# Performance work log

Hardware: AMD Instinct MI355X
Metric: run time of the kernel (lower is better)

Reference implementation:

```python
import jax, jax.numpy as jnp
import numpy as np

M, C, D_EMB, K, LBP_LOOPS, DAMP = 100, 30, 300, 3, 10, 0.5


def setup_inputs() -> dict:
    key = jax.random.key(0)
    k0, k1, k2, k3, k4, k5 = jax.random.split(key, 6)
    ent = jax.random.normal(k0, (M, C, D_EMB), jnp.float32)
    fmc_in = jax.random.normal(k1, (M, 3 * D_EMB), jnp.float32)
    W_fmc = jax.random.normal(k2, (3 * D_EMB, D_EMB), jnp.float32) / np.float32(np.sqrt(3 * D_EMB))
    b_fmc = jnp.zeros((D_EMB,), jnp.float32)
    eye = jnp.eye(D_EMB, dtype=jnp.float32)
    # original init: B, R_k, D_k are identity (diag of ones); add tiny noise so grads are generic
    B = eye + 0.01 * jax.random.normal(k3, (D_EMB, D_EMB), jnp.float32)
    R = eye[None] + 0.01 * jax.random.normal(k4, (K, D_EMB, D_EMB), jnp.float32)
    D = eye[None] + 0.01 * jax.random.normal(k5, (K, D_EMB, D_EMB), jnp.float32)
    return {"ent": ent, "fmc_in": fmc_in, "W_fmc": W_fmc, "b_fmc": b_fmc, "B": B, "R": R, "D": D}


def _lbp(ent, fmc_in, W_fmc, b_fmc, B, R, D):
    # f_m_c: Linear(900,300) + Tanh (dropout off in eval)
    f = jnp.tanh(fmc_in @ W_fmc + b_fmc)                              # [M, d]
    # psi(e, m) = e^T B f_c(m)
    psi = jnp.einsum('mcd,de,me->mc', ent, B, f)                      # [M, C]
    # a_k(m_i, m_j) = softmax_k( f_i^T D_k f_j / sqrt(d) )  (RelNorm)
    s = jnp.einsum('id,kde,je->ijk', f, D, f) / np.float32(np.sqrt(D_EMB))
    a = jax.nn.softmax(s, axis=-1)                                    # [M, M, K]
    # phi_ks(arg, e')_k = arg^T R_k e'  ; arg = candidate q of mention j, e' = candidate p of mention i
    pk = jnp.einsum('jqd,kde,ipe->ijpqk', ent, R, ent)                # [M, M, C, C, K]
    phi = jnp.einsum('ijpqk,ijk->ijpq', pk, a)                        # [M, M, C(e'), C(arg)]

    mbar0 = jnp.zeros((M, M, C), jnp.float32)                         # mbar[i, j, arg-of-j]

    def step(mbar, _):
        stot = mbar.sum(axis=0)                                       # sum_k mbar[k, i, e']  -> [M, C]
        # value(i, j, e'=p, arg=q) = psi(e', i) + phi(arg, e', i, j) + sum_{k != j} mbar[k, i, e']
        vals = (psi[:, None, :, None] + phi
                + stot[:, None, :, None]
                - jnp.transpose(mbar, (1, 0, 2))[:, :, :, None])      # subtract k == j term
        mval = jnp.maximum(0.0, vals.max(axis=2))                     # max over e', maxValue init 0
        # damped update in prob space: log((1-g)*exp(mbar) + g*softmax_arg(mval))
        new = jnp.log((1.0 - DAMP) * jnp.exp(mbar)
                      + DAMP * jax.nn.softmax(mval, axis=-1))
        return new, None

    mbar, _ = jax.lax.scan(step, mbar0, None, length=LBP_LOOPS)

    # ubar[i, arg] = softmax_arg( psi(arg, i) + sum_{k != i} mbar[k, i, arg] )
    u = psi + mbar.sum(axis=0) - jnp.einsum('iic->ic', mbar)
    return jax.nn.softmax(u, axis=-1)                                 # [M, C]


def reference(ent, fmc_in, W_fmc, b_fmc, B, R, D):
    return _lbp(ent, fmc_in, W_fmc, b_fmc, B, R, D)
```

## Files before the change

### kernel.cpp

```cpp
#include <hip/hip_runtime.h>
#include <math.h>

#define MM 100
#define CC 30
#define DE 300
#define NK 3
#define NLOOP 10
#define INV_SQRT_D 0.05773502691896258f

typedef __attribute__((ext_vector_type(8))) short bf16x8;
typedef __attribute__((ext_vector_type(4))) float f32x4;


__device__ inline void bf16split(float x, short* hi, short* lo) {
  unsigned u  = __float_as_uint(x);
  unsigned hu = u & 0xFFFF0000u;
  float xh = __uint_as_float(hu);
  float rl = x - xh;
  unsigned lu = __float_as_uint(rl);
  lu += 0x7FFFu + ((lu >> 16) & 1u);
  *hi = (short)(hu >> 16);
  *lo = (short)(lu >> 16);
}

__global__ __launch_bounds__(256) void k_f1(const float* __restrict__ fmc,
                                            const float* __restrict__ W,
                                            const float* __restrict__ b,
                                            float* __restrict__ f) {
  __shared__ float xs[75];
  const int m  = blockIdx.x / 12;
  const int eq = blockIdx.x % 12;
  const int e0 = eq * 75;
  const int tid = threadIdx.x;
  for (int e = tid; e < 75; e += 256) xs[e] = fmc[m*3*DE + e0 + e];
  __syncthreads();

  const int d0 = tid;
  const int d1 = tid + 256;
  float acc0 = 0.f, acc1 = 0.f;
  for (int e = 0; e < 75; ++e) {
    const float xv = xs[e];
    const float* Wr = W + (e0 + e)*DE;
    acc0 = fmaf(xv, Wr[d0], acc0);
    if (d1 < DE) acc1 = fmaf(xv, Wr[d1], acc1);
  }
  if (eq == 0) {
    acc0 += b[d0];
    if (d1 < DE) acc1 += b[d1];
  }
  atomicAdd(f + m*DE + d0, acc0);
  if (d1 < DE) atomicAdd(f + m*DE + d1, acc1);
}

__global__ void k_tanh(float* __restrict__ f, int n) {
  int idx = blockIdx.x*256 + threadIdx.x;
  if (idx < n) f[idx] = tanhf(f[idx]);
}

__global__ __launch_bounds__(256) void k_gt(const float* __restrict__ Bm,
                                            const float* __restrict__ Dm,
                                            const float* __restrict__ f,
                                            float* __restrict__ gst,
                                            float* __restrict__ t) {
  __shared__ float fs[DE];
  const int m  = blockIdx.x / 19;
  const int cg = blockIdx.x % 19;
  const int wave = threadIdx.x >> 6, lane = threadIdx.x & 63;
  for (int e = threadIdx.x; e < DE; e += 256) fs[e] = f[m*DE + e];
  __syncthreads();

  #pragma unroll
  for (int u = 0; u < 16; ++u) {
    const int col = cg*64 + wave*16 + u;
    const bool ok = (col < 1200);
    const int ccl = ok ? col : 0;
    const float* row = (ccl < DE) ? (Bm + ccl*DE) : (Dm + (ccl - DE)*DE);
    float acc = 0.f;
    for (int e = lane; e < DE; e += 64) acc = fmaf(row[e], fs[e], acc);
    #pragma unroll
    for (int off = 32; off; off >>= 1) acc += __shfl_down(acc, off, 64);
    if (ok && lane == 0) {
      if (col < DE) {
        gst[m*DE + col] = acc;
      } else {
        const int k = (col - DE) / DE, d = (col - DE) % DE;
        t[(k*MM + m)*DE + d] = acc;
      }
    }
  }
}

__global__ __launch_bounds__(256) void k_psi2(const float* __restrict__ ent,
                                              const float* __restrict__ gst,
                                              float* __restrict__ psi) {
  __shared__ float gs[DE];
  const int m  = blockIdx.x >> 3;
  const int cg = blockIdx.x & 7;
  const int wave = threadIdx.x >> 6, lane = threadIdx.x & 63;
  for (int e = threadIdx.x; e < DE; e += 256) gs[e] = gst[m*DE + e];
  __syncthreads();
  const int c = cg*4 + wave;
  if (c < CC) {
    float acc = 0.f;
    const float* er = ent + (m*CC + c)*DE;
    for (int d = lane; d < DE; d += 64) acc = fmaf(er[d], gs[d], acc);
    #pragma unroll
    for (int off = 32; off; off >>= 1) acc += __shfl_down(acc, off, 64);
    if (lane == 0) psi[m*CC + c] = acc;
  }
}

__global__ __launch_bounds__(256) void k_a2(const float* __restrict__ f,
                                            const float* __restrict__ t,
                                            float* __restrict__ a) {
  __shared__ float fs[DE];
  const int i  = blockIdx.x / 25;
  const int jg = blockIdx.x % 25;
  const int wave = threadIdx.x >> 6, lane = threadIdx.x & 63;
  for (int e = threadIdx.x; e < DE; e += 256) fs[e] = f[i*DE + e];
  __syncthreads();
  const int j = jg*4 + wave;
  float sk[NK];
  #pragma unroll
  for (int k = 0; k < NK; ++k) {
    float acc = 0.f;
    const float* tr = t + (k*MM + j)*DE;
    for (int d = lane; d < DE; d += 64) acc = fmaf(fs[d], tr[d], acc);
    #pragma unroll
    for (int off = 32; off; off >>= 1) acc += __shfl_down(acc, off, 64);
    sk[k] = acc;
  }
  if (lane == 0) {
    float s0 = sk[0]*INV_SQRT_D, s1 = sk[1]*INV_SQRT_D, s2 = sk[2]*INV_SQRT_D;
    float mx = fmaxf(s0, fmaxf(s1, s2));
    float e0 = expf(s0 - mx), e1 = expf(s1 - mx), e2 = expf(s2 - mx);
    float inv = 1.f / (e0 + e1 + e2);
    float* ar = a + (i*MM + j)*NK;
    ar[0] = e0*inv; ar[1] = e1*inv; ar[2] = e2*inv;
  }
}

__global__ __launch_bounds__(256) void k_esplit(const float* __restrict__ ent,
                                                short* __restrict__ entH,
                                                short* __restrict__ entL) {
  int j = blockIdx.x;
  for (int idx = threadIdx.x; idx < 32*320; idx += 256) {
    int q = idx / 320, kk = idx % 320;
    float x = (q < CC && kk < DE) ? ent[(j*CC + q)*DE + kk] : 0.f;
    short h, l;
    bf16split(x, &h, &l);
    entH[(j*32 + q)*320 + kk] = h;
    entL[(j*32 + q)*320 + kk] = l;
  }
}

__global__ __launch_bounds__(256) void k_re(const float* __restrict__ R,
                                            const float* __restrict__ ent,
                                            short* __restrict__ REH,
                                            short* __restrict__ REL) {
  __shared__ float4 As4[128*5];
  __shared__ float4 Bs4[64*5];
  float* As = (float*)As4;
  float* Bs = (float*)Bs4;

  const int k  = blockIdx.z;
  const int r0 = blockIdx.y * 128;
  const int d0 = blockIdx.x * 64;
  const int tx = threadIdx.x & 15;
  const int ty = threadIdx.x >> 4;
  const float* A  = ent;
  const float* Bk = R + k*DE*DE;

  float acc[8][4];
  #pragma unroll
  for (int r = 0; r < 8; ++r)
    #pragma unroll
    for (int s = 0; s < 4; ++s) acc[r][s] = 0.f;

  for (int e0 = 0; e0 < DE; e0 += 20) {
    #pragma unroll
    for (int it = 0; it < 10; ++it) {
      int idx = threadIdx.x + it*256;
      int row = idx / 20, e = idx % 20;
      int gr = r0 + row;
      As[idx] = (gr < MM*CC) ? A[gr*DE + e0 + e] : 0.f;
    }
    #pragma unroll
    for (int it = 0; it < 5; ++it) {
      int idx = threadIdx.x + it*256;
      int row = idx / 20, e = idx % 20;
      int gd = d0 + row;
      Bs[idx] = (gd < DE) ? Bk[gd*DE + e0 + e] : 0.f;
    }
    __syncthreads();

    #pragma unroll
    for (int v = 0; v < 5; ++v) {
      float4 av[8], bv[4];
      #pragma unroll
      for (int r = 0; r < 8; ++r) av[r] = As4[(ty + 16*r)*5 + v];
      #pragma unroll
      for (int s = 0; s < 4; ++s) bv[s] = Bs4[(tx + 16*s)*5 + v];
      #pragma unroll
      for (int r = 0; r < 8; ++r)
        #pragma unroll
        for (int s = 0; s < 4; ++s) {
          acc[r][s] = fmaf(av[r].x, bv[s].x, acc[r][s]);
          acc[r][s] = fmaf(av[r].y, bv[s].y, acc[r][s]);
          acc[r][s] = fmaf(av[r].z, bv[s].z, acc[r][s]);
          acc[r][s] = fmaf(av[r].w, bv[s].w, acc[r][s]);
        }
    }
    __syncthreads();
  }

  #pragma unroll
  for (int r = 0; r < 8; ++r) {
    int gr = r0 + ty + 16*r;
    if (gr < MM*CC) {
      int i = gr / CC, p = gr % CC;
      #pragma unroll
      for (int s = 0; s < 4; ++s) {
        int gd = d0 + tx + 16*s;
        if (gd < DE) {
          size_t idx = (((size_t)k*MM + i)*32 + p)*320 + gd;
          short h, l;
          bf16split(acc[r][s], &h, &l);
          REH[idx] = h;
          REL[idx] = l;
        }
      }
    }
  }
}

__global__ __launch_bounds__(256) void k_phi6(const float* __restrict__ a,
                                              const short* __restrict__ REH,
                                              const short* __restrict__ REL,
                                              const short* __restrict__ entH,
                                              const short* __restrict__ entL,
                                              float* __restrict__ phi) {
  __shared__ short As[2][12*512];
  const int bs = blockIdx.x;
  int i, jg;
  if (bs < 2400) {
    int x = bs & 7;
    int s = bs >> 3;
    jg = s / 12;
    i  = x*12 + s % 12;
  } else {
    int r = bs - 2400;
    i  = 96 + (r & 3);
    jg = r >> 2;
  }
  const int wave = threadIdx.x >> 6;
  const int lane = threadIdx.x & 63;
  const int j = jg*4 + wave;

  const int row = lane & 15;
  const int g8  = (lane >> 4) << 3;

  const float a0 = a[(i*MM + j)*NK + 0];
  const float a1 = a[(i*MM + j)*NK + 1];
  const float a2 = a[(i*MM + j)*NK + 2];

  const int b0 = (j*32 + row)*320;
  const int b1 = b0 + 16*320;

  const short* asrc[3];
  short* adst[3];
  #pragma unroll
  for (int q = 0; q < 3; ++q) {
    const int fr = 3*wave + q;
    const int b6 = fr % 6;
    const int kr = b6 >> 1, rb = b6 & 1;
    const short* src = (fr < 6) ? REH : REL;
    asrc[q] = src + ((kr*MM + i)*32 + rb*16 + row)*320 + g8;
    adst[q] = (short*)As + fr*512 + lane*8;
  }

  f32x4 acc[3][2][2];
  #pragma unroll
  for (int kr = 0; kr < 3; ++kr)
    #pragma unroll
    for (int r = 0; r < 2; ++r)
      #pragma unroll
      for (int s = 0; s < 2; ++s)
        acc[kr][r][s] = (f32x4){0.f, 0.f, 0.f, 0.f};

  {
    int4 v0 = *(const int4*)(asrc[0]);
    int4 v1 = *(const int4*)(asrc[1]);
    int4 v2 = *(const int4*)(asrc[2]);
    *(int4*)(adst[0]) = v0;
    *(int4*)(adst[1]) = v1;
    *(int4*)(adst[2]) = v2;
  }
  __syncthreads();

  int cur = 0;
  for (int c = 0; c < 10; ++c) {
    int4 v0, v1, v2;
    if (c < 9) {
      v0 = *(const int4*)(asrc[0] + (c+1)*32);
      v1 = *(const int4*)(asrc[1] + (c+1)*32);
      v2 = *(const int4*)(asrc[2] + (c+1)*32);
    }
    const int kk = c*32 + g8;
    bf16x8 BH0 = *(const bf16x8*)(entH + b0 + kk);
    bf16x8 BH1 = *(const bf16x8*)(entH + b1 + kk);
    bf16x8 BL0 = *(const bf16x8*)(entL + b0 + kk);
    bf16x8 BL1 = *(const bf16x8*)(entL + b1 + kk);

    const short* Ab = (const short*)As + cur*12*512 + lane*8;
    #pragma unroll
    for (int kr = 0; kr < 3; ++kr) {
      bf16x8 AH0 = *(const bf16x8*)(Ab + (kr*2 + 0)*512);
      bf16x8 AH1 = *(const bf16x8*)(Ab + (kr*2 + 1)*512);
      bf16x8 AL0 = *(const bf16x8*)(Ab + (6 + kr*2 + 0)*512);
      bf16x8 AL1 = *(const bf16x8*)(Ab + (6 + kr*2 + 1)*512);
      acc[kr][0][0] = __builtin_amdgcn_mfma_f32_16x16x32_bf16(AH0, BH0, acc[kr][0][0], 0, 0, 0);
      acc[kr][0][0] = __builtin_amdgcn_mfma_f32_16x16x32_bf16(AH0, BL0, acc[kr][0][0], 0, 0, 0);
      acc[kr][0][0] = __builtin_amdgcn_mfma_f32_16x16x32_bf16(AL0, BH0, acc[kr][0][0], 0, 0, 0);
      acc[kr][0][1] = __builtin_amdgcn_mfma_f32_16x16x32_bf16(AH0, BH1, acc[kr][0][1], 0, 0, 0);
      acc[kr][0][1] = __builtin_amdgcn_mfma_f32_16x16x32_bf16(AH0, BL1, acc[kr][0][1], 0, 0, 0);
      acc[kr][0][1] = __builtin_amdgcn_mfma_f32_16x16x32_bf16(AL0, BH1, acc[kr][0][1], 0, 0, 0);
      acc[kr][1][0] = __builtin_amdgcn_mfma_f32_16x16x32_bf16(AH1, BH0, acc[kr][1][0], 0, 0, 0);
      acc[kr][1][0] = __builtin_amdgcn_mfma_f32_16x16x32_bf16(AH1, BL0, acc[kr][1][0], 0, 0, 0);
      acc[kr][1][0] = __builtin_amdgcn_mfma_f32_16x16x32_bf16(AL1, BH0, acc[kr][1][0], 0, 0, 0);
      acc[kr][1][1] = __builtin_amdgcn_mfma_f32_16x16x32_bf16(AH1, BH1, acc[kr][1][1], 0, 0, 0);
      acc[kr][1][1] = __builtin_amdgcn_mfma_f32_16x16x32_bf16(AH1, BL1, acc[kr][1][1], 0, 0, 0);
      acc[kr][1][1] = __builtin_amdgcn_mfma_f32_16x16x32_bf16(AL1, BH1, acc[kr][1][1], 0, 0, 0);
    }

    if (c < 9) {
      short* dst = (short*)As + (cur^1)*12*512;
      *(int4*)(dst + (3*wave + 0)*512 + lane*8) = v0;
      *(int4*)(dst + (3*wave + 1)*512 + lane*8) = v1;
      *(int4*)(dst + (3*wave + 2)*512 + lane*8) = v2;
      __syncthreads();
      cur ^= 1;
    }
  }

  float* ph = phi + (i*MM + j)*CC*CC;
  const int rbase = (lane >> 4) * 4;
  #pragma unroll
  for (int r = 0; r < 2; ++r) {
    #pragma unroll
    for (int t = 0; t < 4; ++t) {
      const int p = 16*r + rbase + t;
      if (p < CC) {
        #pragma unroll
        for (int s = 0; s < 2; ++s) {
          const int q = 16*s + row;
          if (q < CC) {
            float v = a0*acc[0][r][s][t] + a1*acc[1][r][s][t] + a2*acc[2][r][s][t];
            ph[p*CC + q] = v;
          }
        }
      }
    }
  }
}

__global__ void k_zero(float* __restrict__ p, int n) {
  int idx = blockIdx.x*256 + threadIdx.x;
  if (idx < n) p[idx] = 0.f;
}

__global__ __launch_bounds__(256) void k_up4(const float* __restrict__ phi,
                                             const float* __restrict__ psi,
                                             const float* __restrict__ stot_cur,
                                             float* __restrict__ stot_next,
                                             const float* __restrict__ mb_old,
                                             float* __restrict__ mb_new) {
  const int i  = blockIdx.x / 25;
  const int jg = blockIdx.x % 25;
  const int wave = threadIdx.x >> 6;
  const int lane = threadIdx.x & 63;
  const int j = jg*4 + wave;
  const int half = lane >> 5;
  const int q = lane & 31;

  __shared__ float psi_st[32];
  if (threadIdx.x < CC)
    psi_st[threadIdx.x] = psi[i*CC + threadIdx.x] + stot_cur[i*CC + threadIdx.x];
  __syncthreads();

  float csr = (q < CC) ? psi_st[q] - mb_old[(j*MM + i)*CC + q] : -1e30f;

  const float* ph = phi + (i*MM + j)*CC*CC;
  float mv = -1e30f;
  const int p0 = half * 15;
  #pragma unroll
  for (int pp = 0; pp < 15; ++pp) {
    const int p = p0 + pp;
    float v = (q < CC) ? ph[p*CC + q] : -1e30f;
    float cv = __shfl(csr, p, 64);
    mv = fmaxf(mv, v + cv);
  }
  mv = fmaxf(mv, __shfl_xor(mv, 32, 64));
  float x = (q < CC) ? fmaxf(mv, 0.f) : -1e30f;

  float mx = x;
  #pragma unroll
  for (int off = 16; off; off >>= 1) mx = fmaxf(mx, __shfl_xor(mx, off, 64));
  float e = (q < CC) ? expf(x - mx) : 0.f;
  float se = e;
  #pragma unroll
  for (int off = 16; off; off >>= 1) se += __shfl_xor(se, off, 64);

  if (lane < CC) {
    float sm = e / se;
    float old = mb_old[(i*MM + j)*CC + lane];
    float nv = logf(0.5f*expf(old) + 0.5f*sm);
    mb_new[(i*MM + j)*CC + lane] = nv;
    atomicAdd(stot_next + j*CC + lane, nv);
  }
}

__global__ __launch_bounds__(64) void k_final(const float* __restrict__ psi,
                                              const float* __restrict__ stotN,
                                              const float* __restrict__ mb,
                                              float* __restrict__ out) {
  int i = blockIdx.x;
  int lane = threadIdx.x;
  float x = -1e30f;
  if (lane < CC)
    x = psi[i*CC + lane] + stotN[i*CC + lane] - mb[(i*MM + i)*CC + lane];
  float mx = x;
  #pragma unroll
  for (int off = 16; off; off >>= 1) mx = fmaxf(mx, __shfl_xor(mx, off, 32));
  float e = (lane < CC) ? expf(x - mx) : 0.f;
  float se = e;
  #pragma unroll
  for (int off = 16; off; off >>= 1) se += __shfl_xor(se, off, 32);
  if (lane < CC) out[i*CC + lane] = e / se;
}

extern "C" void kernel_launch(void* const* d_in, const int* in_sizes, int n_in,
                              void* d_out, int out_size, void* d_ws, size_t ws_size,
                              hipStream_t stream) {
  (void)in_sizes; (void)n_in; (void)out_size; (void)ws_size;
  const float* ent  = (const float*)d_in[0];
  const float* fmc  = (const float*)d_in[1];
  const float* W    = (const float*)d_in[2];
  const float* b    = (const float*)d_in[3];
  const float* Bm   = (const float*)d_in[4];
  const float* R    = (const float*)d_in[5];
  const float* Dm   = (const float*)d_in[6];
  float* out = (float*)d_out;
  float* ws  = (float*)d_ws;

  float* f    = ws + 0;
  float* psi  = ws + 60000;
  float* t    = ws + 63000;
  float* a    = ws + 153000;
  short* REH  = (short*)(ws + 183000);
  short* REL  = (short*)(ws + 1719000);
  short* entH = (short*)(ws + 3255000);
  short* entL = (short*)(ws + 3767000);
  float* phi  = ws + 4279000;
  float* mbA  = ws + 13279000;
  float* mbB  = ws + 13579000;
  float* stotbuf = ws + 13879000;
  float* gst  = ws + 183000;

  k_zero<<<(633000 + 255)/256, 256, 0, stream>>>(mbA, 633000);
  k_zero<<<(30000 + 255)/256, 256, 0, stream>>>(f, 30000);

  k_f1  <<<1200, 256, 0, stream>>>(fmc, W, b, f);
  k_tanh<<<(30000 + 255)/256, 256, 0, stream>>>(f, 30000);
  k_gt  <<<1900, 256, 0, stream>>>(Bm, Dm, f, gst, t);
  k_psi2<<<MM*8, 256, 0, stream>>>(ent, gst, psi);
  k_a2  <<<MM*25, 256, 0, stream>>>(f, t, a);
  k_esplit<<<MM, 256, 0, stream>>>(ent, entH, entL);

  k_zero<<<(3072000 + 255)/256, 256, 0, stream>>>(ws + 183000, 3072000);
  {
    dim3 grid(5, 24, 3);
    k_re<<<grid, 256, 0, stream>>>(R, ent, REH, REL);
  }
  k_phi6<<<2500, 256, 0, stream>>>(a, REH, REL, entH, entL, phi);

  float* cur = mbA; float* nxt = mbB;
  for (int it = 0; it < NLOOP; ++it) {
    k_up4<<<MM*25, 256, 0, stream>>>(phi, psi,
                                     stotbuf + it*MM*CC,
                                     stotbuf + (it+1)*MM*CC,
                                     cur, nxt);
    float* tmp = cur; cur = nxt; nxt = tmp;
  }
  k_final<<<MM, 64, 0, stream>>>(psi, stotbuf + NLOOP*MM*CC, cur, out);
}
```

Baseline: 447.5 us.

## Fuse LBP iterations into one cooperative kernel with LDS-resident phi tiles

Replaces the ten per-iteration k_up4 launches plus k_final with one persistent cooperative kernel of 512 blocks that uses grid.sync between iterations. Each block loads its 19 phi tiles (about 68 KB) into shared memory once and reuses them across all iterations, so phi is not re-read from global memory every loop. This removes launch overhead and repeated phi traffic, but adds grid-wide barrier cost and relies on cooperative launch occupancy, falling back to the old path if that is unavailable.

Measured after the change: 1.017 ms. 2.27x slower.

```diff
diff --git a/kernel.cpp b/kernel.cpp
--- a/kernel.cpp
+++ b/kernel.cpp
@@ -1,5 +1,8 @@
 #include <hip/hip_runtime.h>
+#include <hip/hip_cooperative_groups.h>
 #include <math.h>
+
+namespace cg = cooperative_groups;
 
 #define MM 100
 #define CC 30
@@ -64,14 +67,14 @@
                                             float* __restrict__ t) {
   __shared__ float fs[DE];
   const int m  = blockIdx.x / 19;
-  const int cg = blockIdx.x % 19;
+  const int cg2 = blockIdx.x % 19;
   const int wave = threadIdx.x >> 6, lane = threadIdx.x & 63;
   for (int e = threadIdx.x; e < DE; e += 256) fs[e] = f[m*DE + e];
   __syncthreads();
 
   #pragma unroll
   for (int u = 0; u < 16; ++u) {
-    const int col = cg*64 + wave*16 + u;
+    const int col = cg2*64 + wave*16 + u;
     const bool ok = (col < 1200);
     const int ccl = ok ? col : 0;
     const float* row = (ccl < DE) ? (Bm + ccl*DE) : (Dm + (ccl - DE)*DE);
@@ -95,11 +98,11 @@
                                               float* __restrict__ psi) {
   __shared__ float gs[DE];
   const int m  = blockIdx.x >> 3;
-  const int cg = blockIdx.x & 7;
+  const int cg2 = blockIdx.x & 7;
   const int wave = threadIdx.x >> 6, lane = threadIdx.x & 63;
   for (int e = threadIdx.x; e < DE; e += 256) gs[e] = gst[m*DE + e];
   __syncthreads();
-  const int c = cg*4 + wave;
+  const int c = cg2*4 + wave;
   if (c < CC) {
     float acc = 0.f;
     const float* er = ent + (m*CC + c)*DE;
@@ -369,6 +372,102 @@
   if (idx < n) p[idx] = 0.f;
 }
 
+__device__ __forceinline__ void lbp_tile(const float* T,
+                                         const float* __restrict__ psi,
+                                         const float* __restrict__ stot_cur,
+                                         float* __restrict__ stot_next,
+                                         const float* __restrict__ mb_old,
+                                         float* __restrict__ mb_new,
+                                         int i, int j, int lane, int half, int q) {
+  float csr = -1e30f;
+  if (q < CC)
+    csr = psi[i*CC + q] + stot_cur[i*CC + q] - mb_old[(j*MM + i)*CC + q];
+
+  float mv = -1e30f;
+  const int p0 = half * 15;
+  #pragma unroll
+  for (int pp = 0; pp < 15; ++pp) {
+    const int p = p0 + pp;
+    float v = (q < CC) ? T[p*CC + q] : -1e30f;
+    float cv = __shfl(csr, p, 64);
+    mv = fmaxf(mv, v + cv);
+  }
+  mv = fmaxf(mv, __shfl_xor(mv, 32, 64));
+  float x = (q < CC) ? fmaxf(mv, 0.f) : -1e30f;
+
+  float mx = x;
+  #pragma unroll
+  for (int off = 16; off; off >>= 1) mx = fmaxf(mx, __shfl_xor(mx, off, 64));
+  float e = (q < CC) ? expf(x - mx) : 0.f;
+  float se = e;
+  #pragma unroll
+  for (int off = 16; off; off >>= 1) se += __shfl_xor(se, off, 64);
+
+  if (lane < CC) {
+    float sm = e / se;
+    float old = mb_old[(i*MM + j)*CC + lane];
+    float nv = logf(0.5f*expf(old) + 0.5f*sm);
+    mb_new[(i*MM + j)*CC + lane] = nv;
+    atomicAdd(stot_next + j*CC + lane, nv);
+  }
+}
+
+__global__ __launch_bounds__(256) void k_loop(const float* __restrict__ phi,
+                                              const float* __restrict__ psi,
+                                              float* __restrict__ stotbuf,
+                                              float* __restrict__ mbA,
+                                              float* __restrict__ mbB,
+                                              float* __restrict__ out) {
+  cg::grid_group grid = cg::this_grid();
+  __shared__ float TL[19*900];
+  const int b = blockIdx.x;
+  const int tid = threadIdx.x;
+  const int wave = tid >> 6, lane = tid & 63;
+  const int half = lane >> 5, q = lane & 31;
+
+  {
+    const size_t base = (size_t)b * (19*900);
+    for (int idx = tid; idx < 19*900; idx += 256) TL[idx] = phi[base + idx];
+  }
+  __syncthreads();
+
+  for (int it = 0; it < NLOOP; ++it) {
+    const float* stot_cur = stotbuf + it*(MM*CC);
+    float* stot_next      = stotbuf + (it+1)*(MM*CC);
+    const float* mb_old = (it & 1) ? mbB : mbA;
+    float*       mb_new = (it & 1) ? mbA : mbB;
+
+    for (int u = wave; u < 20; u += 4) {
+      if (u < 19) {
+        const int tau = b*19 + u;
+        lbp_tile(TL + u*900, psi, stot_cur, stot_next, mb_old, mb_new,
+                 tau / MM, tau % MM, lane, half, q);
+      } else if (b < 272) {
+        const int tau = 9728 + b;
+        lbp_tile(phi + (size_t)tau*900, psi, stot_cur, stot_next, mb_old, mb_new,
+                 tau / MM, tau % MM, lane, half, q);
+      }
+    }
+    grid.sync();
+  }
+
+  if (b < MM && wave == 0) {
+    const float* stotN = stotbuf + NLOOP*(MM*CC);
+    const int i = b;
+    float x = -1e30f;
+    if (lane < CC)
+      x = psi[i*CC + lane] + stotN[i*CC + lane] - mbA[(i*MM + i)*CC + lane];
+    float mx = x;
+    #pragma unroll
+    for (int off = 16; off; off >>= 1) mx = fmaxf(mx, __shfl_xor(mx, off, 32));
+    float e = (lane < CC) ? expf(x - mx) : 0.f;
+    float se = e;
+    #pragma unroll
+    for (int off = 16; off; off >>= 1) se += __shfl_xor(se, off, 32);
+    if (lane < CC) out[i*CC + lane] = e / se;
+  }
+}
+
 __global__ __launch_bounds__(256) void k_up4(const float* __restrict__ phi,
                                              const float* __restrict__ psi,
                                              const float* __restrict__ stot_cur,
@@ -382,42 +481,8 @@
   const int j = jg*4 + wave;
   const int half = lane >> 5;
   const int q = lane & 31;
-
-  __shared__ float psi_st[32];
-  if (threadIdx.x < CC)
-    psi_st[threadIdx.x] = psi[i*CC + threadIdx.x] + stot_cur[i*CC + threadIdx.x];
-  __syncthreads();
-
-  float csr = (q < CC) ? psi_st[q] - mb_old[(j*MM + i)*CC + q] : -1e30f;
-
-  const float* ph = phi + (i*MM + j)*CC*CC;
-  float mv = -1e30f;
-  const int p0 = half * 15;
-  #pragma unroll
-  for (int pp = 0; pp < 15; ++pp) {
-    const int p = p0 + pp;
-    float v = (q < CC) ? ph[p*CC + q] : -1e30f;
-    float cv = __shfl(csr, p, 64);
-    mv = fmaxf(mv, v + cv);
-  }
-  mv = fmaxf(mv, __shfl_xor(mv, 32, 64));
-  float x = (q < CC) ? fmaxf(mv, 0.f) : -1e30f;
-
-  float mx = x;
-  #pragma unroll
-  for (int off = 16; off; off >>= 1) mx = fmaxf(mx, __shfl_xor(mx, off, 64));
-  float e = (q < CC) ? expf(x - mx) : 0.f;
-  float se = e;
-  #pragma unroll
-  for (int off = 16; off; off >>= 1) se += __shfl_xor(se, off, 64);
-
-  if (lane < CC) {
-    float sm = e / se;
-    float old = mb_old[(i*MM + j)*CC + lane];
-    float nv = logf(0.5f*expf(old) + 0.5f*sm);
-    mb_new[(i*MM + j)*CC + lane] = nv;
-    atomicAdd(stot_next + j*CC + lane, nv);
-  }
+  lbp_tile(phi + (size_t)(i*MM + j)*CC*CC, psi, stot_cur, stot_next,
+           mb_old, mb_new, i, j, lane, half, q);
 }
 
 __global__ __launch_bounds__(64) void k_final(const float* __restrict__ psi,
@@ -484,13 +549,30 @@
   }
   k_phi6<<<2500, 256, 0, stream>>>(a, REH, REL, entH, entL, phi);
 
-  float* cur = mbA; float* nxt = mbB;
-  for (int it = 0; it < NLOOP; ++it) {
-    k_up4<<<MM*25, 256, 0, stream>>>(phi, psi,
-                                     stotbuf + it*MM*CC,
-                                     stotbuf + (it+1)*MM*CC,
-                                     cur, nxt);
-    float* tmp = cur; cur = nxt; nxt = tmp;
-  }
-  k_final<<<MM, 64, 0, stream>>>(psi, stotbuf + NLOOP*MM*CC, cur, out);
-}
+  bool coop = false;
+  {
+    int maxB = 0, nCU = 0, dev = 0;
+    if (hipGetDevice(&dev) == hipSuccess &&
+        hipOccupancyMaxActiveBlocksPerMultiprocessor(&maxB, k_loop, 256, 0) == hipSuccess &&
+        hipDeviceGetAttribute(&nCU, hipDeviceAttributeMultiprocessorCount, dev) == hipSuccess)
+      coop = (maxB >= 1 && (long)maxB * nCU >= 512);
+  }
+  if (coop) {
+    void* args[] = {(void*)&phi, (void*)&psi, (void*)&stotbuf,
+                    (void*)&mbA, (void*)&mbB, (void*)&out};
+    hipError_t e = hipLaunchCooperativeKernel((void*)k_loop, dim3(512), dim3(256),
+                                              args, 0, stream);
+    if (e != hipSuccess) coop = false;
+  }
+  if (!coop) {
+    float* cur = mbA; float* nxt = mbB;
+    for (int it = 0; it < NLOOP; ++it) {
+      k_up4<<<MM*25, 256, 0, stream>>>(phi, psi,
+                                       stotbuf + it*MM*CC,
+                                       stotbuf + (it+1)*MM*CC,
+                                       cur, nxt);
+      float* tmp = cur; cur = nxt; nxt = tmp;
+    }
+    k_final<<<MM, 64, 0, stream>>>(psi, stotbuf + NLOOP*MM*CC, cur, out);
+  }
+}
```
